# Optimization experiments

Measured on AMD Instinct MI355X. Metric: run time of the kernel, lower is better.

Reference implementation:

```python
import jax, jax.numpy as jnp
import numpy as np

N_NODES = 50000


def _gcn_conv(x, edge_list, edge_attr, W, b):
    # PyG GCNConv with edge_weight: add self loops (weight 1), symmetric norm,
    # h = x @ W, out[dst] += norm * h[src], then + bias.
    n = x.shape[0]
    src, dst = edge_list[0], edge_list[1]
    loop = jnp.arange(n)
    src_f = jnp.concatenate([src, loop])
    dst_f = jnp.concatenate([dst, loop])
    w_f = jnp.concatenate([edge_attr, jnp.ones((n,), dtype=x.dtype)])
    deg = jax.ops.segment_sum(w_f, dst_f, num_segments=n)
    dinv = jnp.where(deg > 0, jax.lax.rsqrt(jnp.where(deg > 0, deg, 1.0)), 0.0)
    norm = dinv[src_f] * w_f * dinv[dst_f]          # [E+N]
    h = x @ W                                        # [N, 64]
    msg = h[src_f] * norm[:, None]                   # [E+N, 64] gather
    out = jax.ops.segment_sum(msg, dst_f, num_segments=n)  # scatter-add
    return out + b


def setup_inputs() -> dict:
    key = jax.random.key(0)
    k1, k2, k3, k4, k5 = jax.random.split(key, 5)
    N, E, F, H = N_NODES, 1_600_000, 128, 64
    x = jax.random.normal(k1, (N, F), dtype=jnp.float32)
    edge_list = jax.random.randint(k2, (2, E), 0, N, dtype=jnp.int64)
    edge_attr = jax.random.uniform(k3, (E,), dtype=jnp.float32)
    conv_w = jax.random.normal(k4, (F, H), dtype=jnp.float32) * (1.0 / np.sqrt(F))
    conv_b = jnp.zeros((H,), dtype=jnp.float32)
    fc_w = jax.random.normal(k5, (N * H,), dtype=jnp.float32) * (1.0 / np.sqrt(N * H))
    fc_b = jnp.zeros((1,), dtype=jnp.float32)
    return {"x": x, "edge_list": edge_list, "edge_attr": edge_attr,
            "conv_w": conv_w, "conv_b": conv_b, "fc_w": fc_w, "fc_b": fc_b}


def reference(x, edge_list, edge_attr, conv_w, conv_b, fc_w, fc_b):
    # training=False: gaussian noise and dropout are no-ops
    h = _gcn_conv(x, edge_list, edge_attr, conv_w, conv_b)
    h = jax.nn.relu(h)
    flat = h.reshape(-1)                       # [N*64]
    logit = jnp.dot(flat, fc_w) + fc_b[0]      # scalar
    return jax.nn.sigmoid(logit)
```

## Files before the change

kernel.cpp:

```cpp
#include <hip/hip_runtime.h>
#include <hip/hip_bf16.h>
#include <math.h>

constexpr int F = 128;
constexpr int H = 64;
constexpr int NB = 32;
constexpr int XS_STRIDE = F + 4;

#define MASK40 ((1ull << 40) - 1)
#define Q24 16777216.0f

__device__ __forceinline__ float blo(unsigned u) { return __uint_as_float(u << 16); }
__device__ __forceinline__ float bhi(unsigned u) { return __uint_as_float(u & 0xffff0000u); }

__global__ __launch_bounds__(256) void k_init(unsigned long long* __restrict__ pk,
                                              float* __restrict__ gacc,
                                              unsigned int* __restrict__ done, int N) {
  int i = blockIdx.x * 256 + threadIdx.x;
  if (i < N) pk[i] = 0ull;
  if (i == 0) { gacc[0] = 0.0f; done[0] = 0u; }
}

__global__ __launch_bounds__(256) void k_mix(const float* __restrict__ x,
                                             const float* __restrict__ W,
                                             unsigned short* __restrict__ hb, int N,
                                             const int* __restrict__ dst,
                                             const float* __restrict__ w,
                                             unsigned long long* __restrict__ pk,
                                             int* __restrict__ rank, int E, int G) {
  __shared__ float Ws[F * H];
  __shared__ float xs[NB * XS_STRIDE];
  if ((int)blockIdx.x >= G) {
    int e = ((int)blockIdx.x - G) * 256 + threadIdx.x;
    if (e < E) {
      int d = dst[e];
      unsigned long long enc =
          (1ull << 40) | (unsigned long long)__float2uint_rn(w[e] * Q24);
      unsigned long long old = atomicAdd(&pk[d], enc);
      rank[e] = (int)(old >> 40);
    }
    return;
  }
  const int t = threadIdx.x;
  {
    const float4* W4 = (const float4*)W;
    float4* Ws4 = (float4*)Ws;
#pragma unroll
    for (int i = 0; i < (F * H / 4) / 256; ++i) Ws4[t + i * 256] = W4[t + i * 256];
  }
  const int node0 = blockIdx.x * NB;
  {
    const float4* x4 = (const float4*)(x + (size_t)node0 * F);
    int lim = (N - node0 < NB ? N - node0 : NB) * (F / 4);
    for (int i = t; i < NB * (F / 4); i += 256) {
      int nl = i / (F / 4), kk = i % (F / 4);
      float4 v = (i < lim) ? x4[i] : make_float4(0.f, 0.f, 0.f, 0.f);
      *(float4*)&xs[nl * XS_STRIDE + kk * 4] = v;
    }
  }
  __syncthreads();
  const int f0 = (t & 15) * 4;
  const int nl0 = (t >> 4) * 2;
  float acc[2][4] = {};
  for (int k = 0; k < F; k += 4) {
    float xr[2][4];
    float wr[4][4];
    *(float4*)&xr[0][0] = *(const float4*)&xs[(nl0 + 0) * XS_STRIDE + k];
    *(float4*)&xr[1][0] = *(const float4*)&xs[(nl0 + 1) * XS_STRIDE + k];
#pragma unroll
    for (int i = 0; i < 4; ++i)
      *(float4*)&wr[i][0] = *(const float4*)&Ws[(k + i) * H + f0];
#pragma unroll
    for (int i = 0; i < 4; ++i)
#pragma unroll
      for (int n = 0; n < 2; ++n)
#pragma unroll
        for (int j = 0; j < 4; ++j)
          acc[n][j] += xr[n][i] * wr[i][j];
  }
#pragma unroll
  for (int n = 0; n < 2; ++n) {
    int node = node0 + nl0 + n;
    if (node < N) {
      ushort4 o;
      o.x = __bfloat16_as_ushort(__float2bfloat16(acc[n][0]));
      o.y = __bfloat16_as_ushort(__float2bfloat16(acc[n][1]));
      o.z = __bfloat16_as_ushort(__float2bfloat16(acc[n][2]));
      o.w = __bfloat16_as_ushort(__float2bfloat16(acc[n][3]));
      *(ushort4*)&hb[(size_t)node * H + f0] = o;
    }
  }
}

__global__ __launch_bounds__(1024) void k_scan1(const unsigned long long* __restrict__ pk,
                                                int* __restrict__ cnt,
                                                float* __restrict__ dinv,
                                                int* __restrict__ cursor,
                                                int* __restrict__ bsum, int N) {
  __shared__ int buf[1024];
  const int t = threadIdx.x;
  const int i = blockIdx.x * 1024 + t;
  int v = 0;
  if (i < N) {
    unsigned long long p = pk[i];
    v = (int)(p >> 40);
    cnt[i] = v;
    dinv[i] = rsqrtf(1.0f + (float)(p & MASK40) * (1.0f / Q24));
  }
  buf[t] = v;
  __syncthreads();
  for (int off = 1; off < 1024; off <<= 1) {
    int add = (t >= off) ? buf[t - off] : 0;
    __syncthreads();
    buf[t] += add;
    __syncthreads();
  }
  if (i < N) cursor[i] = buf[t] - v;
  if (t == 1023) bsum[blockIdx.x] = buf[t];
}

__global__ void k_scan2(const int* __restrict__ bsum, int* __restrict__ bpre, int B) {
  if (threadIdx.x == 0) {
    int run = 0;
    for (int b = 0; b < B; ++b) { bpre[b] = run; run += bsum[b]; }
  }
}

__global__ __launch_bounds__(256) void k_fill(const int* __restrict__ src,
                                              const int* __restrict__ dst,
                                              const float* __restrict__ w,
                                              const int* __restrict__ rank,
                                              const float* __restrict__ dinv,
                                              const int* __restrict__ cursor,
                                              const int* __restrict__ bpre,
                                              int2* __restrict__ sorted, int E) {
  int e = blockIdx.x * 256 + threadIdx.x;
  if (e < E) {
    int d = dst[e];
    int s = src[e];
    float sw = dinv[s] * w[e];
    int pos = cursor[d] + bpre[d >> 10] + rank[e];
    sorted[pos] = make_int2(s, __float_as_int(sw));
  }
}

__global__ __launch_bounds__(256) void k_agg(const int2* __restrict__ sorted,
                                             const int* __restrict__ cursor,
                                             const int* __restrict__ bpre,
                                             const int* __restrict__ cnt,
                                             const float* __restrict__ dinv,
                                             const unsigned short* __restrict__ hb,
                                             const float* __restrict__ b,
                                             const float* __restrict__ fcw,
                                             float* __restrict__ gacc,
                                             unsigned int* __restrict__ done,
                                             const float* __restrict__ fcb,
                                             float* __restrict__ out,
                                             int N, int nBlocks) {
  const int wid = threadIdx.x >> 6;
  const int lane = threadIdx.x & 63;
  const int seg = lane >> 3;
  const int sl = lane & 7;
  const int n = blockIdx.x * 32 + wid * 8 + seg;
  const uint4* h4 = (const uint4*)hb;
  float p = 0.0f;
  if (n < N) {
    float dn = dinv[n];
    float dn2 = dn * dn;
    uint4 rn = h4[(size_t)n * 8 + sl];
    float4 b0 = ((const float4*)b)[sl * 2];
    float4 b1 = ((const float4*)b)[sl * 2 + 1];
    float a0 = b0.x + dn2 * blo(rn.x), a1 = b0.y + dn2 * bhi(rn.x);
    float a2 = b0.z + dn2 * blo(rn.y), a3 = b0.w + dn2 * bhi(rn.y);
    float a4 = b1.x + dn2 * blo(rn.z), a5 = b1.y + dn2 * bhi(rn.z);
    float a6 = b1.z + dn2 * blo(rn.w), a7 = b1.w + dn2 * bhi(rn.w);
    int e = cursor[n] + bpre[n >> 10];
    int end = e + cnt[n];
    for (; e + 1 < end; e += 2) {
      int2 e0 = sorted[e];
      int2 e1 = sorted[e + 1];
      uint4 r0 = h4[(size_t)e0.x * 8 + sl];
      uint4 r1 = h4[(size_t)e1.x * 8 + sl];
      float n0 = dn * __int_as_float(e0.y);
      float n1 = dn * __int_as_float(e1.y);
      a0 += n0 * blo(r0.x) + n1 * blo(r1.x);
      a1 += n0 * bhi(r0.x) + n1 * bhi(r1.x);
      a2 += n0 * blo(r0.y) + n1 * blo(r1.y);
      a3 += n0 * bhi(r0.y) + n1 * bhi(r1.y);
      a4 += n0 * blo(r0.z) + n1 * blo(r1.z);
      a5 += n0 * bhi(r0.z) + n1 * bhi(r1.z);
      a6 += n0 * blo(r0.w) + n1 * blo(r1.w);
      a7 += n0 * bhi(r0.w) + n1 * bhi(r1.w);
    }
    if (e < end) {
      int2 e0 = sorted[e];
      uint4 r0 = h4[(size_t)e0.x * 8 + sl];
      float n0 = dn * __int_as_float(e0.y);
      a0 += n0 * blo(r0.x); a1 += n0 * bhi(r0.x);
      a2 += n0 * blo(r0.y); a3 += n0 * bhi(r0.y);
      a4 += n0 * blo(r0.z); a5 += n0 * bhi(r0.z);
      a6 += n0 * blo(r0.w); a7 += n0 * bhi(r0.w);
    }
    float4 f0 = ((const float4*)fcw)[(size_t)n * 16 + sl * 2];
    float4 f1 = ((const float4*)fcw)[(size_t)n * 16 + sl * 2 + 1];
    p = fmaxf(a0, 0.f) * f0.x + fmaxf(a1, 0.f) * f0.y +
        fmaxf(a2, 0.f) * f0.z + fmaxf(a3, 0.f) * f0.w +
        fmaxf(a4, 0.f) * f1.x + fmaxf(a5, 0.f) * f1.y +
        fmaxf(a6, 0.f) * f1.z + fmaxf(a7, 0.f) * f1.w;
  }
  p += __shfl_down(p, 4);
  p += __shfl_down(p, 2);
  p += __shfl_down(p, 1);
  __shared__ float ls[32];
  if (sl == 0) ls[wid * 8 + seg] = p;
  __syncthreads();
  if (threadIdx.x == 0) {
    float s = 0.f;
#pragma unroll
    for (int i = 0; i < 32; ++i) s += ls[i];
    atomicAdd(gacc, s);
    __threadfence();
    unsigned int ticket = atomicAdd(done, 1u);
    if (ticket == (unsigned int)(nBlocks - 1)) {
      float tot = atomicAdd(gacc, 0.0f);
      float logit = tot + fcb[0];
      out[0] = 1.0f / (1.0f + expf(-logit));
    }
  }
}

extern "C" void kernel_launch(void* const* d_in, const int* in_sizes, int n_in,
                              void* d_out, int out_size, void* d_ws, size_t ws_size,
                              hipStream_t stream) {
  const float* x      = (const float*)d_in[0];
  const int*   elist  = (const int*)d_in[1];
  const float* eattr  = (const float*)d_in[2];
  const float* conv_w = (const float*)d_in[3];
  const float* conv_b = (const float*)d_in[4];
  const float* fc_w   = (const float*)d_in[5];
  const float* fc_b   = (const float*)d_in[6];
  float* out = (float*)d_out;

  const int N = in_sizes[0] / F;
  const int E = in_sizes[2];
  const int* src = elist;
  const int* dst = elist + E;

  char* wsb = (char*)d_ws;
  int2*  sorted = (int2*)wsb;
  unsigned long long* pk = (unsigned long long*)(wsb + (size_t)E * 8);
  int*   rank   = (int*)(pk + N);
  unsigned short* hb = (unsigned short*)(rank + E);
  int*   cnt    = (int*)(hb + (size_t)N * H);
  int*   cursor = cnt + N;
  float* dinv   = (float*)(cursor + N);
  const int nScan = (N + 1023) / 1024;
  int*   bsum   = (int*)(dinv + N);
  int*   bpre   = bsum + nScan;
  float* gacc   = (float*)(bpre + nScan);
  unsigned int* done = (unsigned int*)(gacc + 1);

  const int G = (N + NB - 1) / NB;
  const int C = (E + 255) / 256;
  const int nAgg = (N + 31) / 32;

  k_init<<<(N + 255) / 256, 256, 0, stream>>>(pk, gacc, done, N);
  k_mix<<<G + C, 256, 0, stream>>>(x, conv_w, hb, N, dst, eattr, pk, rank, E, G);
  k_scan1<<<nScan, 1024, 0, stream>>>(pk, cnt, dinv, cursor, bsum, N);
  k_scan2<<<1, 64, 0, stream>>>(bsum, bpre, nScan);
  k_fill<<<(E + 255) / 256, 256, 0, stream>>>(src, dst, eattr, rank, dinv, cursor,
                                              bpre, sorted, E);
  k_agg<<<nAgg, 256, 0, stream>>>(sorted, cursor, bpre, cnt, dinv, hb, conv_b, fc_w,
                                  gacc, done, fc_b, out, N, nAgg);
}
```

Baseline: 285.7 us.

## Split mixed count/GEMM kernel, fold block-sum scan into consumers, unroll aggregation by four

The combined GEMM/edge-count kernel is split into two separate launches. The single-thread block-prefix kernel is removed, and each fill and aggregation block now recomputes the 64-entry block prefix with wavefront shuffles. The aggregation loop aligns to even edge indices, reads two packed edges per 16-byte load, processes four neighbours per iteration, and applies the dn scaling once at the end. These changes are meant to cut one launch, remove a serial scan, and increase memory-level parallelism in the gather. The price is an extra launch from the split, redundant per-block scans, and the scan only handling up to 64 block sums (N up to 65536).

```diff
diff --git a/kernel.cpp b/kernel.cpp
--- a/kernel.cpp
+++ b/kernel.cpp
@@ -21,26 +21,25 @@
   if (i == 0) { gacc[0] = 0.0f; done[0] = 0u; }
 }
 
-__global__ __launch_bounds__(256) void k_mix(const float* __restrict__ x,
-                                             const float* __restrict__ W,
-                                             unsigned short* __restrict__ hb, int N,
-                                             const int* __restrict__ dst,
-                                             const float* __restrict__ w,
-                                             unsigned long long* __restrict__ pk,
-                                             int* __restrict__ rank, int E, int G) {
+__global__ __launch_bounds__(256) void k_count(const int* __restrict__ dst,
+                                               const float* __restrict__ w,
+                                               unsigned long long* __restrict__ pk,
+                                               int* __restrict__ rank, int E) {
+  int e = blockIdx.x * 256 + threadIdx.x;
+  if (e < E) {
+    int d = dst[e];
+    unsigned long long enc =
+        (1ull << 40) | (unsigned long long)__float2uint_rn(w[e] * Q24);
+    unsigned long long old = atomicAdd(&pk[d], enc);
+    rank[e] = (int)(old >> 40);
+  }
+}
+
+__global__ __launch_bounds__(256) void k_gemm(const float* __restrict__ x,
+                                              const float* __restrict__ W,
+                                              unsigned short* __restrict__ hb, int N) {
   __shared__ float Ws[F * H];
   __shared__ float xs[NB * XS_STRIDE];
-  if ((int)blockIdx.x >= G) {
-    int e = ((int)blockIdx.x - G) * 256 + threadIdx.x;
-    if (e < E) {
-      int d = dst[e];
-      unsigned long long enc =
-          (1ull << 40) | (unsigned long long)__float2uint_rn(w[e] * Q24);
-      unsigned long long old = atomicAdd(&pk[d], enc);
-      rank[e] = (int)(old >> 40);
-    }
-    return;
-  }
   const int t = threadIdx.x;
   {
     const float4* W4 = (const float4*)W;
@@ -119,11 +118,20 @@
   if (t == 1023) bsum[blockIdx.x] = buf[t];
 }
 
-__global__ void k_scan2(const int* __restrict__ bsum, int* __restrict__ bpre, int B) {
-  if (threadIdx.x == 0) {
-    int run = 0;
-    for (int b = 0; b < B; ++b) { bpre[b] = run; run += bsum[b]; }
-  }
+__device__ __forceinline__ void scan_bsum(const int* __restrict__ bsum, int nScan,
+                                          int* bp) {
+  const int t = threadIdx.x;
+  if (t < 64) {
+    int v = (t < nScan) ? bsum[t] : 0;
+    int orig = v;
+#pragma unroll
+    for (int off = 1; off < 64; off <<= 1) {
+      int u = __shfl_up(v, off);
+      if (t >= off) v += u;
+    }
+    bp[t] = v - orig;
+  }
+  __syncthreads();
 }
 
 __global__ __launch_bounds__(256) void k_fill(const int* __restrict__ src,
@@ -132,21 +140,23 @@
                                               const int* __restrict__ rank,
                                               const float* __restrict__ dinv,
                                               const int* __restrict__ cursor,
-                                              const int* __restrict__ bpre,
+                                              const int* __restrict__ bsum, int nScan,
                                               int2* __restrict__ sorted, int E) {
+  __shared__ int bp[64];
+  scan_bsum(bsum, nScan, bp);
   int e = blockIdx.x * 256 + threadIdx.x;
   if (e < E) {
     int d = dst[e];
     int s = src[e];
     float sw = dinv[s] * w[e];
-    int pos = cursor[d] + bpre[d >> 10] + rank[e];
+    int pos = cursor[d] + bp[d >> 10] + rank[e];
     sorted[pos] = make_int2(s, __float_as_int(sw));
   }
 }
 
 __global__ __launch_bounds__(256) void k_agg(const int2* __restrict__ sorted,
                                              const int* __restrict__ cursor,
-                                             const int* __restrict__ bpre,
+                                             const int* __restrict__ bsum, int nScan,
                                              const int* __restrict__ cnt,
                                              const float* __restrict__ dinv,
                                              const unsigned short* __restrict__ hb,
@@ -157,6 +167,8 @@
                                              const float* __restrict__ fcb,
                                              float* __restrict__ out,
                                              int N, int nBlocks) {
+  __shared__ int bp[64];
+  scan_bsum(bsum, nScan, bp);
   const int wid = threadIdx.x >> 6;
   const int lane = threadIdx.x & 63;
   const int seg = lane >> 3;
@@ -165,42 +177,61 @@
   const uint4* h4 = (const uint4*)hb;
   float p = 0.0f;
   if (n < N) {
+    float a0 = 0.f, a1 = 0.f, a2 = 0.f, a3 = 0.f;
+    float a4 = 0.f, a5 = 0.f, a6 = 0.f, a7 = 0.f;
+    uint4 rn = h4[(size_t)n * 8 + sl];
+    int e = cursor[n] + bp[n >> 10];
+    int end = e + cnt[n];
+    if (e < end && (e & 1)) {
+      int2 e0 = sorted[e];
+      uint4 r0 = h4[(size_t)e0.x * 8 + sl];
+      float s0 = __int_as_float(e0.y);
+      a0 += s0 * blo(r0.x); a1 += s0 * bhi(r0.x);
+      a2 += s0 * blo(r0.y); a3 += s0 * bhi(r0.y);
+      a4 += s0 * blo(r0.z); a5 += s0 * bhi(r0.z);
+      a6 += s0 * blo(r0.w); a7 += s0 * bhi(r0.w);
+      ++e;
+    }
+    const int4* s4 = (const int4*)sorted;
+    for (; e + 3 < end; e += 4) {
+      int4 ea = s4[e >> 1];
+      int4 eb = s4[(e >> 1) + 1];
+      uint4 r0 = h4[(size_t)ea.x * 8 + sl];
+      uint4 r1 = h4[(size_t)ea.z * 8 + sl];
+      uint4 r2 = h4[(size_t)eb.x * 8 + sl];
+      uint4 r3 = h4[(size_t)eb.z * 8 + sl];
+      float s0 = __int_as_float(ea.y), s1 = __int_as_float(ea.w);
+      float s2 = __int_as_float(eb.y), s3 = __int_as_float(eb.w);
+      a0 += s0 * blo(r0.x) + s1 * blo(r1.x) + s2 * blo(r2.x) + s3 * blo(r3.x);
+      a1 += s0 * bhi(r0.x) + s1 * bhi(r1.x) + s2 * bhi(r2.x) + s3 * bhi(r3.x);
+      a2 += s0 * blo(r0.y) + s1 * blo(r1.y) + s2 * blo(r2.y) + s3 * blo(r3.y);
+      a3 += s0 * bhi(r0.y) + s1 * bhi(r1.y) + s2 * bhi(r2.y) + s3 * bhi(r3.y);
+      a4 += s0 * blo(r0.z) + s1 * blo(r1.z) + s2 * blo(r2.z) + s3 * blo(r3.z);
+      a5 += s0 * bhi(r0.z) + s1 * bhi(r1.z) + s2 * bhi(r2.z) + s3 * bhi(r3.z);
+      a6 += s0 * blo(r0.w) + s1 * blo(r1.w) + s2 * blo(r2.w) + s3 * blo(r3.w);
+      a7 += s0 * bhi(r0.w) + s1 * bhi(r1.w) + s2 * bhi(r2.w) + s3 * bhi(r3.w);
+    }
+    for (; e < end; ++e) {
+      int2 e0 = sorted[e];
+      uint4 r0 = h4[(size_t)e0.x * 8 + sl];
+      float s0 = __int_as_float(e0.y);
+      a0 += s0 * blo(r0.x); a1 += s0 * bhi(r0.x);
+      a2 += s0 * blo(r0.y); a3 += s0 * bhi(r0.y);
+      a4 += s0 * blo(r0.z); a5 += s0 * bhi(r0.z);
+      a6 += s0 * blo(r0.w); a7 += s0 * bhi(r0.w);
+    }
     float dn = dinv[n];
     float dn2 = dn * dn;
-    uint4 rn = h4[(size_t)n * 8 + sl];
     float4 b0 = ((const float4*)b)[sl * 2];
     float4 b1 = ((const float4*)b)[sl * 2 + 1];
-    float a0 = b0.x + dn2 * blo(rn.x), a1 = b0.y + dn2 * bhi(rn.x);
-    float a2 = b0.z + dn2 * blo(rn.y), a3 = b0.w + dn2 * bhi(rn.y);
-    float a4 = b1.x + dn2 * blo(rn.z), a5 = b1.y + dn2 * bhi(rn.z);
-    float a6 = b1.z + dn2 * blo(rn.w), a7 = b1.w + dn2 * bhi(rn.w);
-    int e = cursor[n] + bpre[n >> 10];
-    int end = e + cnt[n];
-    for (; e + 1 < end; e += 2) {
-      int2 e0 = sorted[e];
-      int2 e1 = sorted[e + 1];
-      uint4 r0 = h4[(size_t)e0.x * 8 + sl];
-      uint4 r1 = h4[(size_t)e1.x * 8 + sl];
-      float n0 = dn * __int_as_float(e0.y);
-      float n1 = dn * __int_as_float(e1.y);
-      a0 += n0 * blo(r0.x) + n1 * blo(r1.x);
-      a1 += n0 * bhi(r0.x) + n1 * bhi(r1.x);
-      a2 += n0 * blo(r0.y) + n1 * blo(r1.y);
-      a3 += n0 * bhi(r0.y) + n1 * bhi(r1.y);
-      a4 += n0 * blo(r0.z) + n1 * blo(r1.z);
-      a5 += n0 * bhi(r0.z) + n1 * bhi(r1.z);
-      a6 += n0 * blo(r0.w) + n1 * blo(r1.w);
-      a7 += n0 * bhi(r0.w) + n1 * bhi(r1.w);
-    }
-    if (e < end) {
-      int2 e0 = sorted[e];
-      uint4 r0 = h4[(size_t)e0.x * 8 + sl];
-      float n0 = dn * __int_as_float(e0.y);
-      a0 += n0 * blo(r0.x); a1 += n0 * bhi(r0.x);
-      a2 += n0 * blo(r0.y); a3 += n0 * bhi(r0.y);
-      a4 += n0 * blo(r0.z); a5 += n0 * bhi(r0.z);
-      a6 += n0 * blo(r0.w); a7 += n0 * bhi(r0.w);
-    }
+    a0 = b0.x + dn2 * blo(rn.x) + dn * a0;
+    a1 = b0.y + dn2 * bhi(rn.x) + dn * a1;
+    a2 = b0.z + dn2 * blo(rn.y) + dn * a2;
+    a3 = b0.w + dn2 * bhi(rn.y) + dn * a3;
+    a4 = b1.x + dn2 * blo(rn.z) + dn * a4;
+    a5 = b1.y + dn2 * bhi(rn.z) + dn * a5;
+    a6 = b1.z + dn2 * blo(rn.w) + dn * a6;
+    a7 = b1.w + dn2 * bhi(rn.w) + dn * a7;
     float4 f0 = ((const float4*)fcw)[(size_t)n * 16 + sl * 2];
     float4 f1 = ((const float4*)fcw)[(size_t)n * 16 + sl * 2 + 1];
     p = fmaxf(a0, 0.f) * f0.x + fmaxf(a1, 0.f) * f0.y +
@@ -256,20 +287,17 @@
   float* dinv   = (float*)(cursor + N);
   const int nScan = (N + 1023) / 1024;
   int*   bsum   = (int*)(dinv + N);
-  int*   bpre   = bsum + nScan;
-  float* gacc   = (float*)(bpre + nScan);
+  float* gacc   = (float*)(bsum + 64);
   unsigned int* done = (unsigned int*)(gacc + 1);
 
-  const int G = (N + NB - 1) / NB;
-  const int C = (E + 255) / 256;
   const int nAgg = (N + 31) / 32;
 
   k_init<<<(N + 255) / 256, 256, 0, stream>>>(pk, gacc, done, N);
-  k_mix<<<G + C, 256, 0, stream>>>(x, conv_w, hb, N, dst, eattr, pk, rank, E, G);
+  k_count<<<(E + 255) / 256, 256, 0, stream>>>(dst, eattr, pk, rank, E);
+  k_gemm<<<(N + NB - 1) / NB, 256, 0, stream>>>(x, conv_w, hb, N);
   k_scan1<<<nScan, 1024, 0, stream>>>(pk, cnt, dinv, cursor, bsum, N);
-  k_scan2<<<1, 64, 0, stream>>>(bsum, bpre, nScan);
   k_fill<<<(E + 255) / 256, 256, 0, stream>>>(src, dst, eattr, rank, dinv, cursor,
-                                              bpre, sorted, E);
-  k_agg<<<nAgg, 256, 0, stream>>>(sorted, cursor, bpre, cnt, dinv, hb, conv_b, fc_w,
-                                  gacc, done, fc_b, out, N, nAgg);
-}
+                                              bsum, nScan, sorted, E);
+  k_agg<<<nAgg, 256, 0, stream>>>(sorted, cursor, bsum, nScan, cnt, dinv, hb,
+                                  conv_b, fc_w, gacc, done, fc_b, out, N, nAgg);
+}
```

After: 291.0 us. No clear change (+1.9%).
